# Performance work log

Hardware: AMD Instinct MI355X
Metric: run time of the kernel (lower is better)

Reference implementation:

```python
import jax, jax.numpy as jnp
import numpy as np


def setup_inputs() -> dict:
    key = jax.random.key(0)
    ks = jax.random.split(key, 8)
    B, N, H = 8, 64, 256
    nE, E = 256, 64
    HID, OUT = 512, 1
    s1 = 1.0 / np.sqrt(H + E)
    s2 = 1.0 / np.sqrt(HID)
    return {
        "h_all": jax.random.normal(ks[0], (B, N, H), dtype=jnp.float32),
        "e_feat": jax.random.normal(ks[1], (nE, E), dtype=jnp.float32),
        "W1": jax.random.normal(ks[2], (H + E, HID), dtype=jnp.float32) * s1,
        "b1": jnp.zeros((HID,), dtype=jnp.float32),
        "W2": jax.random.normal(ks[3], (HID, HID), dtype=jnp.float32) * s2,
        "b2": jnp.zeros((HID,), dtype=jnp.float32),
        "W3": jax.random.normal(ks[4], (HID, OUT), dtype=jnp.float32) * s2,
        "b3": jnp.zeros((OUT,), dtype=jnp.float32),
    }


def reference(h_all, e_feat, W1, b1, W2, b2, W3, b3):
    # Math == MLP(cat([expand(h), expand(e)], -1)) but computed via split
    # weights: cat([h,e]) @ W1 == h @ W1[:H] + e @ W1[H:], avoiding the
    # materialized [B,N,nE,H+E] concat tensor.
    H = h_all.shape[-1]
    Wh, We = W1[:H], W1[H:]
    h_part = jnp.einsum("bnh,hk->bnk", h_all, Wh)        # [B,N,HID]
    e_part = jnp.einsum("ed,dk->ek", e_feat, We)          # [nE,HID]
    x = h_part[:, :, None, :] + e_part[None, None, :, :] + b1  # [B,N,nE,HID]
    x = jax.nn.relu(x)
    x = jax.nn.relu(jnp.einsum("bnek,kj->bnej", x, W2) + b2)
    return jnp.einsum("bnek,ko->bneo", x, W3) + b3        # [B,N,nE,OUT]
```

## Files before the change

kernel.cpp:

```cpp
#include <hip/hip_runtime.h>
#include <hip/hip_bf16.h>


typedef __attribute__((ext_vector_type(8))) short bf16x8;
typedef __attribute__((ext_vector_type(4))) float f32x4;

static __device__ __forceinline__ ushort2 pk_bf16(float a, float b) {
  union { __hip_bfloat162 h; ushort2 u; } c;
  c.h = __float22bfloat162_rn(make_float2(a, b));
  return c.u;
}
static __device__ __forceinline__ float bf2f(unsigned short u) {
  union { unsigned int i; float f; } c;
  c.i = ((unsigned int)u) << 16;
  return c.f;
}

__global__ __launch_bounds__(256) void k_prep(
    const float* __restrict__ h_all, const float* __restrict__ e_feat,
    const float* __restrict__ W1, const float* __restrict__ b1,
    const float* __restrict__ W2,
    unsigned short* __restrict__ hpb, unsigned short* __restrict__ epb,
    unsigned short* __restrict__ w2f) {
  __shared__ float sm[64 * 68];
  const int t = threadIdx.x;
  const int b = blockIdx.x;

  if (b < 256) {
    const int r0 = b * 2;
    float (*hs)[256] = (float(*)[256])sm;
    hs[0][t] = h_all[(size_t)r0 * 256 + t];
    hs[1][t] = h_all[(size_t)(r0 + 1) * 256 + t];
    __syncthreads();
    float2 a0 = make_float2(0.f, 0.f), a1 = make_float2(0.f, 0.f);
    #pragma unroll 2
    for (int k = 0; k < 256; k += 4) {
      float2 w0 = *(const float2*)(W1 + (size_t)k * 512 + 2 * t);
      float2 w1 = *(const float2*)(W1 + (size_t)(k + 1) * 512 + 2 * t);
      float2 w2v = *(const float2*)(W1 + (size_t)(k + 2) * 512 + 2 * t);
      float2 w3v = *(const float2*)(W1 + (size_t)(k + 3) * 512 + 2 * t);
      float h00 = hs[0][k], h01 = hs[0][k + 1], h02 = hs[0][k + 2], h03 = hs[0][k + 3];
      float h10 = hs[1][k], h11 = hs[1][k + 1], h12 = hs[1][k + 2], h13 = hs[1][k + 3];
      a0.x = fmaf(h00, w0.x, a0.x); a0.y = fmaf(h00, w0.y, a0.y);
      a1.x = fmaf(h10, w0.x, a1.x); a1.y = fmaf(h10, w0.y, a1.y);
      a0.x = fmaf(h01, w1.x, a0.x); a0.y = fmaf(h01, w1.y, a0.y);
      a1.x = fmaf(h11, w1.x, a1.x); a1.y = fmaf(h11, w1.y, a1.y);
      a0.x = fmaf(h02, w2v.x, a0.x); a0.y = fmaf(h02, w2v.y, a0.y);
      a1.x = fmaf(h12, w2v.x, a1.x); a1.y = fmaf(h12, w2v.y, a1.y);
      a0.x = fmaf(h03, w3v.x, a0.x); a0.y = fmaf(h03, w3v.y, a0.y);
      a1.x = fmaf(h13, w3v.x, a1.x); a1.y = fmaf(h13, w3v.y, a1.y);
    }
    float2 bv = *(const float2*)(b1 + 2 * t);
    *(ushort2*)(hpb + (size_t)r0 * 512 + 2 * t) = pk_bf16(a0.x + bv.x, a0.y + bv.y);
    *(ushort2*)(hpb + (size_t)(r0 + 1) * 512 + 2 * t) = pk_bf16(a1.x + bv.x, a1.y + bv.y);
  } else if (b < 288) {
    const int r0 = (b - 256) * 8;
    sm[t] = e_feat[(size_t)r0 * 64 + t];
    sm[256 + t] = e_feat[(size_t)r0 * 64 + 256 + t];
    __syncthreads();
    float2 acc[8];
    #pragma unroll
    for (int i = 0; i < 8; ++i) acc[i] = make_float2(0.f, 0.f);
    for (int k = 0; k < 64; ++k) {
      float2 wv = *(const float2*)(W1 + (size_t)(256 + k) * 512 + 2 * t);
      #pragma unroll
      for (int i = 0; i < 8; ++i) {
        acc[i].x = fmaf(sm[i * 64 + k], wv.x, acc[i].x);
        acc[i].y = fmaf(sm[i * 64 + k], wv.y, acc[i].y);
      }
    }
    #pragma unroll
    for (int i = 0; i < 8; ++i)
      *(ushort2*)(epb + (size_t)(r0 + i) * 512 + 2 * t) = pk_bf16(acc[i].x, acc[i].y);
  } else {
    const int bb = b - 288;
    const int k0 = (bb >> 3) * 64;
    const int c0 = (bb & 7) * 64;
    #pragma unroll
    for (int rr = 0; rr < 4; ++rr) {
      const int row = rr * 16 + (t >> 4);
      float4 v = *(const float4*)(W2 + (size_t)(k0 + row) * 512 + c0 + (t & 15) * 4);
      *(float4*)(&sm[row * 68 + (t & 15) * 4]) = v;
    }
    __syncthreads();
    #pragma unroll
    for (int s2 = 0; s2 < 2; ++s2) {
      const int s = t * 2 + s2;
      const int rec = s >> 6, l = s & 63;
      const int jg = (c0 >> 4) + (rec & 3);
      const int ksg = (k0 >> 5) + (rec >> 2);
      const int cl = (rec & 3) * 16 + (l & 15);
      const int kl = (rec >> 2) * 32 + (l >> 4) * 8;
      union { ushort2 o[4]; uint4 v; } u;
      #pragma unroll
      for (int uu = 0; uu < 4; ++uu)
        u.o[uu] = pk_bf16(sm[(kl + 2 * uu) * 68 + cl], sm[(kl + 2 * uu + 1) * 68 + cl]);
      *(uint4*)(w2f + ((size_t)(jg * 16 + ksg) * 64 + l) * 8) = u.v;
    }
  }
}

__global__ __launch_bounds__(256, 2) void k_main(
    const unsigned short* __restrict__ hpb, const unsigned short* __restrict__ epb,
    const unsigned short* __restrict__ w2f, const float* __restrict__ b2,
    const float* __restrict__ W3, const float* __restrict__ b3,
    float* __restrict__ out) {
  __shared__ unsigned short x1s[64 * 512];

  const int t = threadIdx.x;
  const int lane = t & 63;
  const int w = t >> 6;
  const int l15 = lane & 15, l4 = lane >> 4;
  const int bn = blockIdx.x >> 2;
  const int e0 = (blockIdx.x & 3) << 6;
  const int off = (blockIdx.x * 11) & 15;
  const unsigned short* hprow = hpb + (size_t)bn * 512;

  const unsigned short* wrec = w2f + (size_t)w * 65536 + (size_t)lane * 8;
  bf16x8 bb[2][8];
  #pragma unroll
  for (int j = 0; j < 8; ++j) {
    bb[0][j] = *(const bf16x8*)(wrec + j * 8192 + (size_t)off * 512);
    bb[1][j] = *(const bf16x8*)(wrec + j * 8192 + (size_t)((off + 1) & 15) * 512);
  }

  {
    const unsigned short* eprow = epb + (size_t)(e0 + w * 16 + l15) * 512;
    #pragma unroll 4
    for (int ksi = 0; ksi < 16; ++ksi) {
      const int k0 = ksi * 32 + l4 * 8;
      union { uint4 v; unsigned short s[8]; } hv, ev, ov;
      hv.v = *(const uint4*)(hprow + k0);
      ev.v = *(const uint4*)(eprow + k0);
      #pragma unroll
      for (int u = 0; u < 4; ++u) {
        ushort2 p = pk_bf16(fmaxf(bf2f(hv.s[2 * u]) + bf2f(ev.s[2 * u]), 0.f),
                            fmaxf(bf2f(hv.s[2 * u + 1]) + bf2f(ev.s[2 * u + 1]), 0.f));
        ov.s[2 * u] = p.x;
        ov.s[2 * u + 1] = p.y;
      }
      *(uint4*)(&x1s[(size_t)(w * 16 + ksi) * 512 + lane * 8]) = ov.v;
    }
  }
  __syncthreads();

  bf16x8 af[2][4];
  #pragma unroll
  for (int i = 0; i < 4; ++i)
    af[0][i] = *(const bf16x8*)(&x1s[(size_t)(i * 16 + off) * 512 + lane * 8]);

  f32x4 acc[4][8] = {};
  #pragma unroll 4
  for (int ks = 0; ks < 16; ++ks) {
    const int cur = ks & 1;
    const int nxt = cur ^ 1;
    const int kra = (ks + 1 + off) & 15;
    const int krb = (ks + 2 + off) & 15;
    #pragma unroll
    for (int j = 0; j < 8; ++j) {
      #pragma unroll
      for (int i = 0; i < 4; ++i)
        acc[i][j] = __builtin_amdgcn_mfma_f32_16x16x32_bf16(af[cur][i], bb[cur][j], acc[i][j], 0, 0, 0);
      bb[cur][j] = *(const bf16x8*)(wrec + j * 8192 + (size_t)krb * 512);
      if (j < 4)
        af[nxt][j] = *(const bf16x8*)(&x1s[(size_t)(j * 16 + kra) * 512 + lane * 8]);
    }
  }

  float part[16];
  #pragma unroll
  for (int u = 0; u < 16; ++u) part[u] = 0.f;
  #pragma unroll
  for (int j = 0; j < 8; ++j) {
    const int n = w * 128 + j * 16 + l15;
    const float b2v = b2[n], w3v = W3[n];
    #pragma unroll
    for (int i = 0; i < 4; ++i)
      #pragma unroll
      for (int r = 0; r < 4; ++r)
        part[i * 4 + r] = fmaf(fmaxf(acc[i][j][r] + b2v, 0.f), w3v, part[i * 4 + r]);
  }
  #pragma unroll
  for (int u = 0; u < 16; ++u) {
    float v = part[u];
    v += __shfl_xor(v, 1);
    v += __shfl_xor(v, 2);
    v += __shfl_xor(v, 4);
    v += __shfl_xor(v, 8);
    part[u] = v;
  }
  __syncthreads();
  float* osum = (float*)x1s;
  if (l15 == 0) {
    #pragma unroll
    for (int i = 0; i < 4; ++i)
      #pragma unroll
      for (int r = 0; r < 4; ++r)
        osum[w * 64 + i * 16 + l4 * 4 + r] = part[i * 4 + r];
  }
  __syncthreads();
  if (t < 64) {
    float s = b3[0] + osum[t] + osum[64 + t] + osum[128 + t] + osum[192 + t];
    out[(size_t)bn * 256 + e0 + t] = s;
  }
}

extern "C" void kernel_launch(void* const* d_in, const int* in_sizes, int n_in,
                              void* d_out, int out_size, void* d_ws, size_t ws_size,
                              hipStream_t stream) {
  const float* h_all  = (const float*)d_in[0];
  const float* e_feat = (const float*)d_in[1];
  const float* W1     = (const float*)d_in[2];
  const float* b1     = (const float*)d_in[3];
  const float* W2     = (const float*)d_in[4];
  const float* b2     = (const float*)d_in[5];
  const float* W3     = (const float*)d_in[6];
  const float* b3     = (const float*)d_in[7];
  float* out = (float*)d_out;

  unsigned short* hpb = (unsigned short*)d_ws;
  unsigned short* epb = hpb + 512 * 512;
  unsigned short* w2f = epb + 256 * 512;

  hipLaunchKernelGGL(k_prep, dim3(352), dim3(256), 0, stream,
                     h_all, e_feat, W1, b1, W2, hpb, epb, w2f);
  hipLaunchKernelGGL(k_main, dim3(2048), dim3(256), 0, stream,
                     hpb, epb, w2f, b2, W3, b3, out);
}
```

Before: 157.3 us.

## Double k_main block to 128 edge rows with 8 waves in a 2x4 grid

```diff
diff --git a/kernel.cpp b/kernel.cpp
--- a/kernel.cpp
+++ b/kernel.cpp
@@ -100,35 +100,36 @@
   }
 }
 
-__global__ __launch_bounds__(256, 2) void k_main(
+__global__ __launch_bounds__(512, 2) void k_main(
     const unsigned short* __restrict__ hpb, const unsigned short* __restrict__ epb,
     const unsigned short* __restrict__ w2f, const float* __restrict__ b2,
     const float* __restrict__ W3, const float* __restrict__ b3,
     float* __restrict__ out) {
-  __shared__ unsigned short x1s[64 * 512];
+  __shared__ unsigned short x1s[128 * 512];
 
   const int t = threadIdx.x;
   const int lane = t & 63;
   const int w = t >> 6;
   const int l15 = lane & 15, l4 = lane >> 4;
-  const int bn = blockIdx.x >> 2;
-  const int e0 = (blockIdx.x & 3) << 6;
-  const int off = (blockIdx.x * 11) & 15;
+  const int rg = w >> 2;
+  const int cg = w & 3;
+  const int bn = blockIdx.x >> 1;
+  const int e0 = (blockIdx.x & 1) << 7;
   const unsigned short* hprow = hpb + (size_t)bn * 512;
 
-  const unsigned short* wrec = w2f + (size_t)w * 65536 + (size_t)lane * 8;
+  const unsigned short* wrec = w2f + (size_t)cg * 65536 + (size_t)lane * 8;
   bf16x8 bb[2][8];
   #pragma unroll
   for (int j = 0; j < 8; ++j) {
-    bb[0][j] = *(const bf16x8*)(wrec + j * 8192 + (size_t)off * 512);
-    bb[1][j] = *(const bf16x8*)(wrec + j * 8192 + (size_t)((off + 1) & 15) * 512);
+    bb[0][j] = *(const bf16x8*)(wrec + j * 8192);
+    bb[1][j] = *(const bf16x8*)(wrec + j * 8192 + 512);
   }
 
   {
     const unsigned short* eprow = epb + (size_t)(e0 + w * 16 + l15) * 512;
     #pragma unroll 4
-    for (int ksi = 0; ksi < 16; ++ksi) {
-      const int k0 = ksi * 32 + l4 * 8;
+    for (int ks = 0; ks < 16; ++ks) {
+      const int k0 = ks * 32 + l4 * 8;
       union { uint4 v; unsigned short s[8]; } hv, ev, ov;
       hv.v = *(const uint4*)(hprow + k0);
       ev.v = *(const uint4*)(eprow + k0);
@@ -139,32 +140,28 @@
         ov.s[2 * u] = p.x;
         ov.s[2 * u + 1] = p.y;
       }
-      *(uint4*)(&x1s[(size_t)(w * 16 + ksi) * 512 + lane * 8]) = ov.v;
+      *(uint4*)(&x1s[(size_t)(w * 16 + ks) * 512 + lane * 8]) = ov.v;
     }
   }
   __syncthreads();
-
-  bf16x8 af[2][4];
-  #pragma unroll
-  for (int i = 0; i < 4; ++i)
-    af[0][i] = *(const bf16x8*)(&x1s[(size_t)(i * 16 + off) * 512 + lane * 8]);
 
   f32x4 acc[4][8] = {};
   #pragma unroll 4
   for (int ks = 0; ks < 16; ++ks) {
     const int cur = ks & 1;
-    const int nxt = cur ^ 1;
-    const int kra = (ks + 1 + off) & 15;
-    const int krb = (ks + 2 + off) & 15;
-    #pragma unroll
-    for (int j = 0; j < 8; ++j) {
-      #pragma unroll
-      for (int i = 0; i < 4; ++i)
-        acc[i][j] = __builtin_amdgcn_mfma_f32_16x16x32_bf16(af[cur][i], bb[cur][j], acc[i][j], 0, 0, 0);
+    const int krb = (ks + 2) & 15;
+    bf16x8 a[4];
+    #pragma unroll
+    for (int i = 0; i < 4; ++i)
+      a[i] = *(const bf16x8*)(&x1s[(size_t)(((rg * 4 + i) * 16) + ks) * 512 + lane * 8]);
+    #pragma unroll
+    for (int i = 0; i < 4; ++i)
+      #pragma unroll
+      for (int j = 0; j < 8; ++j)
+        acc[i][j] = __builtin_amdgcn_mfma_f32_16x16x32_bf16(a[i], bb[cur][j], acc[i][j], 0, 0, 0);
+    #pragma unroll
+    for (int j = 0; j < 8; ++j)
       bb[cur][j] = *(const bf16x8*)(wrec + j * 8192 + (size_t)krb * 512);
-      if (j < 4)
-        af[nxt][j] = *(const bf16x8*)(&x1s[(size_t)(j * 16 + kra) * 512 + lane * 8]);
-    }
   }
 
   float part[16];
@@ -172,7 +169,7 @@
   for (int u = 0; u < 16; ++u) part[u] = 0.f;
   #pragma unroll
   for (int j = 0; j < 8; ++j) {
-    const int n = w * 128 + j * 16 + l15;
+    const int n = cg * 128 + j * 16 + l15;
     const float b2v = b2[n], w3v = W3[n];
     #pragma unroll
     for (int i = 0; i < 4; ++i)
@@ -196,11 +193,11 @@
     for (int i = 0; i < 4; ++i)
       #pragma unroll
       for (int r = 0; r < 4; ++r)
-        osum[w * 64 + i * 16 + l4 * 4 + r] = part[i * 4 + r];
+        osum[cg * 128 + rg * 64 + i * 16 + l4 * 4 + r] = part[i * 4 + r];
   }
   __syncthreads();
-  if (t < 64) {
-    float s = b3[0] + osum[t] + osum[64 + t] + osum[128 + t] + osum[192 + t];
+  if (t < 128) {
+    float s = b3[0] + osum[t] + osum[128 + t] + osum[256 + t] + osum[384 + t];
     out[(size_t)bn * 256 + e0 + t] = s;
   }
 }
@@ -224,6 +221,6 @@
 
   hipLaunchKernelGGL(k_prep, dim3(352), dim3(256), 0, stream,
                      h_all, e_feat, W1, b1, W2, hpb, epb, w2f);
-  hipLaunchKernelGGL(k_main, dim3(2048), dim3(256), 0, stream,
+  hipLaunchKernelGGL(k_main, dim3(1024), dim3(512), 0, stream,
                      hpb, epb, w2f, b2, W3, b3, out);
 }
```

Measured after the change: 160.4 us. No clear change (+2.0%).
